# Kernel optimization log

Measured on AMD Instinct MI355X. Metric: run time of the kernel, lower is better.

## Reference

```python
import jax, jax.numpy as jnp
import numpy as np

NUM_TOKENS = 8192
EMBED_DIM = 32
BETA = 1.0
DECAY = 0.99
L2_EPS = 1e-12  # torch F.normalize denom clamp


def l2norm(t):
    return t / jnp.maximum(jnp.linalg.norm(t, axis=-1, keepdims=True), L2_EPS)


def setup_inputs() -> dict:
    key = jax.random.key(0)
    k1, k2 = jax.random.split(key)
    z = jax.random.normal(k1, (32, EMBED_DIM, 16, 16), dtype=jnp.float32)  # [B, C, H, W]
    embedding = l2norm(jax.random.normal(k2, (NUM_TOKENS, EMBED_DIM), dtype=jnp.float32))
    cluster_sizes = jnp.zeros((NUM_TOKENS,), dtype=jnp.float32)
    return {"z": z, "embedding": embedding, "cluster_sizes": cluster_sizes}


def reference(z, embedding, cluster_sizes):
    B, C, H, W = z.shape
    zc = jnp.transpose(z, (0, 2, 3, 1))          # channel_last: [B, H, W, C]
    zn = l2norm(zc)
    z_flat = zn.reshape(-1, C)                   # [N, C], N = B*H*W

    # nearest centroid by cosine similarity (codebook rows are unit norm)
    cos_sim = z_flat @ embedding.T               # [N, K]
    token_ids = jnp.argmax(cos_sim, axis=-1)     # [N]
    z_q_flat = embedding[token_ids]              # gather, [N, C]
    z_q = z_q_flat.reshape(zn.shape)

    # EMA statistics (training branch; one-hot @ matmuls expressed as scatter-adds)
    bins = jnp.zeros((NUM_TOKENS,), z.dtype).at[token_ids].add(1.0)      # encodings.sum(0)
    new_cluster_sizes = cluster_sizes * DECAY + (1.0 - DECAY) * bins
    zero_mask = bins == 0
    bins_c = jnp.where(zero_mask, 1.0, bins)
    embed_sum = jnp.zeros((NUM_TOKENS, C), z.dtype).at[token_ids].add(z_flat)  # (z_flat.T @ onehot).T
    embed_normalized = l2norm(embed_sum / bins_c[:, None])
    embed_normalized = jnp.where(zero_mask[:, None], embedding, embed_normalized)
    new_embedding = l2norm(embedding * DECAY + (1.0 - DECAY) * embed_normalized)

    # commitment loss + straight-through estimator
    loss = BETA * jnp.mean((jax.lax.stop_gradient(z_q) - zn) ** 2)
    z_q_st = zn + jax.lax.stop_gradient(z_q - zn)
    z_q_out = jnp.transpose(z_q_st, (0, 3, 1, 2))  # back to [B, C, H, W]

    return (z_q_out, loss, token_ids.reshape(B, H, W), new_embedding, new_cluster_sizes)
```

## Files before the change

### kernel.cpp

```cpp
#include <hip/hip_runtime.h>


#define NTOK   8192
#define NCODE  8192
#define CDIM   32
#define HW     256
#define DECAYF 0.99f
#define EPSF   0.01f

#define OUT_ZQ   0
#define OUT_LOSS 262144
#define OUT_IDS  262145
#define OUT_EMB  270337
#define OUT_CS   532481

#define WS_ZN     0u
#define WS_ZNBF   1048576u
#define WS_EBF    1572864u
#define WS_PMAX   2097152u
#define WS_PACK   3145728u

#define CHUNK  256
#define NCHUNK (NCODE / CHUNK)
#define TILES  (CHUNK / 16)

typedef __attribute__((ext_vector_type(8))) short bf16x8;
typedef __attribute__((ext_vector_type(4))) float f32x4;

__device__ inline unsigned short f2bf(float x) {
    unsigned u = __float_as_uint(x);
    return (unsigned short)((u + 0x7FFFu + ((u >> 16) & 1u)) >> 16);
}
__device__ inline unsigned fmap(float s) {
    unsigned u = __float_as_uint(s);
    return (u & 0x80000000u) ? ~u : (u | 0x80000000u);
}

__device__ inline void stage_chunk(const unsigned short* __restrict__ ebf,
                                   int kbase, float4* lbs5, int t) {
    const float4* src = (const float4*)(ebf + (size_t)kbase * CDIM);
#pragma unroll
    for (int j = 0; j < 4; ++j) {
        int u = t + j * 256;
        int row = u >> 2, seg = u & 3;
        lbs5[row * 5 + seg] = src[u];
    }
}

__global__ __launch_bounds__(256) void k_prep(const float* __restrict__ z,
                                              const float* __restrict__ emb,
                                              float* __restrict__ zn,
                                              unsigned short* __restrict__ znbf,
                                              unsigned short* __restrict__ ebf,
                                              unsigned long long* __restrict__ packed,
                                              float* __restrict__ out) {
    int bid = blockIdx.x, t = threadIdx.x;
    if (bid < 32) {
        int n = bid * 256 + t;
        int b = n >> 8, hw = n & 255;
        const float* zp = z + (size_t)b * (CDIM * HW) + hw;
        float v[CDIM];
        float ss = 0.f;
#pragma unroll
        for (int c = 0; c < CDIM; ++c) {
            float tv = zp[c * HW];
            v[c] = tv;
            ss += tv * tv;
        }
        float d = fmaxf(sqrtf(ss), 1e-12f);
        float* o = zn + (size_t)n * CDIM;
        unsigned short* ob = znbf + (size_t)n * CDIM;
#pragma unroll
        for (int c = 0; c < CDIM; ++c) {
            float tv = v[c] / d;
            o[c] = tv;
            ob[c] = f2bf(tv);
        }
    } else if (bid < 160) {
        int base = (bid - 32) * 2048 + t * 8;
        const float4* s = (const float4*)(emb + base);
        float4 x4 = s[0], y4 = s[1];
        ushort4 u0 = {f2bf(x4.x), f2bf(x4.y), f2bf(x4.z), f2bf(x4.w)};
        ushort4 u1 = {f2bf(y4.x), f2bf(y4.y), f2bf(y4.z), f2bf(y4.w)};
        *(ushort4*)(ebf + base) = u0;
        *(ushort4*)(ebf + base + 4) = u1;
    } else if (bid < 164) {
        int base = (bid - 160) * 2048 + t;
#pragma unroll
        for (int j = 0; j < 8; ++j) packed[base + j * 256] = 0ull;
    } else {
        if (t == 0) out[OUT_LOSS] = 0.f;
    }
}

__global__ __launch_bounds__(256) void k_max(const unsigned short* __restrict__ znbf,
                                             const unsigned short* __restrict__ ebf,
                                             float* __restrict__ pmax) {
    __shared__ float4 lbs5[CHUNK * 5];
    __shared__ float lmax[256];
    int kbase = blockIdx.y * CHUNK;
    stage_chunk(ebf, kbase, lbs5, threadIdx.x);
    __syncthreads();

    int wave = threadIdx.x >> 6, lane = threadIdx.x & 63;
    int col = lane & 15, quad = lane >> 4;
    int wtok = blockIdx.x * 256 + wave * 64;

    bf16x8 a[4];
#pragma unroll
    for (int f = 0; f < 4; ++f)
        a[f] = *(const bf16x8*)(znbf + (size_t)(wtok + f * 16 + col) * CDIM + quad * 8);

    const bf16x8* bl = (const bf16x8*)lbs5;
    const f32x4 zero4 = {0.f, 0.f, 0.f, 0.f};
    float m[4][4];
#pragma unroll
    for (int f = 0; f < 4; ++f)
#pragma unroll
        for (int r = 0; r < 4; ++r) m[f][r] = -1e30f;

    for (int t = 0; t < TILES; ++t) {
        bf16x8 b = bl[(t * 16 + col) * 5 + quad];
#pragma unroll
        for (int f = 0; f < 4; ++f) {
            f32x4 d = __builtin_amdgcn_mfma_f32_16x16x32_bf16(a[f], b, zero4, 0, 0, 0);
#pragma unroll
            for (int r = 0; r < 4; ++r) m[f][r] = fmaxf(m[f][r], d[r]);
        }
    }
#pragma unroll
    for (int f = 0; f < 4; ++f)
#pragma unroll
        for (int r = 0; r < 4; ++r) {
            float v = m[f][r];
#pragma unroll
            for (int s = 1; s < 16; s <<= 1) v = fmaxf(v, __shfl_xor(v, s));
            if (col == 0) lmax[wave * 64 + f * 16 + quad * 4 + r] = v;
        }
    __syncthreads();
    pmax[(size_t)blockIdx.y * NTOK + blockIdx.x * 256 + threadIdx.x] = lmax[threadIdx.x];
}

__global__ __launch_bounds__(256, 4) void k_pick(const float* __restrict__ zn,
                                                 const float* __restrict__ emb,
                                                 const float* __restrict__ pmax,
                                                 unsigned long long* __restrict__ packed) {
    __shared__ int qlist[256];
    __shared__ int qcnt;
    int t = threadIdx.x, lane = t & 63;
    int x = blockIdx.x, y = blockIdx.y;
    int code = y * CHUNK + t;

    if (t == 0) qcnt = 0;

    const float4* ef = (const float4*)(emb + (size_t)code * CDIM);
    float4 e0 = ef[0], e1 = ef[1], e2 = ef[2], e3 = ef[3];
    float4 e4 = ef[4], e5 = ef[5], e6 = ef[6], e7 = ef[7];

    int tok = x * 256 + t;
    float mx = -1e30f, pmy = -1e30f;
#pragma unroll
    for (int ch = 0; ch < NCHUNK; ++ch) {
        float p = pmax[(size_t)ch * NTOK + tok];
        if (ch == y) pmy = p;
        mx = fmaxf(mx, p);
    }
    __syncthreads();
    if (pmy >= mx - EPSF) qlist[atomicAdd(&qcnt, 1)] = t;
    __syncthreads();
    int nq = qcnt;

    for (int i = 0; i < nq; ++i) {
        int tl = __builtin_amdgcn_readfirstlane(qlist[i]);
        int n = x * 256 + tl;
        const float* zp = zn + (size_t)n * CDIM;
        float a0 = zp[0] * e0.x, a1 = zp[1] * e0.y;
        float a2 = zp[2] * e0.z, a3 = zp[3] * e0.w;
        a0 = __builtin_fmaf(zp[4], e1.x, a0);  a1 = __builtin_fmaf(zp[5], e1.y, a1);
        a2 = __builtin_fmaf(zp[6], e1.z, a2);  a3 = __builtin_fmaf(zp[7], e1.w, a3);
        a0 = __builtin_fmaf(zp[8], e2.x, a0);  a1 = __builtin_fmaf(zp[9], e2.y, a1);
        a2 = __builtin_fmaf(zp[10], e2.z, a2); a3 = __builtin_fmaf(zp[11], e2.w, a3);
        a0 = __builtin_fmaf(zp[12], e3.x, a0); a1 = __builtin_fmaf(zp[13], e3.y, a1);
        a2 = __builtin_fmaf(zp[14], e3.z, a2); a3 = __builtin_fmaf(zp[15], e3.w, a3);
        a0 = __builtin_fmaf(zp[16], e4.x, a0); a1 = __builtin_fmaf(zp[17], e4.y, a1);
        a2 = __builtin_fmaf(zp[18], e4.z, a2); a3 = __builtin_fmaf(zp[19], e4.w, a3);
        a0 = __builtin_fmaf(zp[20], e5.x, a0); a1 = __builtin_fmaf(zp[21], e5.y, a1);
        a2 = __builtin_fmaf(zp[22], e5.z, a2); a3 = __builtin_fmaf(zp[23], e5.w, a3);
        a0 = __builtin_fmaf(zp[24], e6.x, a0); a1 = __builtin_fmaf(zp[25], e6.y, a1);
        a2 = __builtin_fmaf(zp[26], e6.z, a2); a3 = __builtin_fmaf(zp[27], e6.w, a3);
        a0 = __builtin_fmaf(zp[28], e7.x, a0); a1 = __builtin_fmaf(zp[29], e7.y, a1);
        a2 = __builtin_fmaf(zp[30], e7.z, a2); a3 = __builtin_fmaf(zp[31], e7.w, a3);
        float s = (a0 + a1) + (a2 + a3);
        unsigned long long key = ((unsigned long long)fmap(s) << 13) |
                                 (unsigned long long)(8191 - code);
#pragma unroll
        for (int sh = 1; sh < 64; sh <<= 1) {
            unsigned long long o = __shfl_xor(key, sh);
            if (o > key) key = o;
        }
        if (lane == 0) atomicMax(packed + n, key);
    }
}

__global__ __launch_bounds__(256) void k_final(const unsigned long long* __restrict__ packed,
                                               const float* __restrict__ zn,
                                               const float* __restrict__ emb,
                                               const float* __restrict__ cs,
                                               float* __restrict__ out) {
    __shared__ float lesum[32][32];
    __shared__ int lbins[32];
    __shared__ int lsid[32];
    __shared__ float ls4[4];

    int blk = blockIdx.x, t = threadIdx.x;
    int wave = t >> 6, lane = t & 63;
    int tok0 = blk * 32, kbase = blk * 32;

    if (t < 32) lbins[t] = 0;
#pragma unroll
    for (int i = 0; i < 4; ++i) {
        int idx = i * 256 + t;
        lesum[idx >> 5][idx & 31] = 0.f;
    }
    if (t < 32) {
        int n = tok0 + t;
        int id = 8191 - (int)(packed[n] & 8191ull);
        lsid[t] = id;
        out[OUT_IDS + n] = (float)id;
    }
    __syncthreads();

    float s = 0.f;
#pragma unroll
    for (int i = 0; i < 4; ++i) {
        int idx = i * 256 + t;
        int tl = idx >> 5, c = idx & 31;
        int n = tok0 + tl;
        int id = lsid[tl];
        float ev = emb[(size_t)id * CDIM + c];
        float zv = zn[(size_t)n * CDIM + c];
        int b = n >> 8, hw = n & 255;
        out[OUT_ZQ + ((size_t)b * CDIM + c) * HW + hw] = ev;
        float dd = ev - zv;
        s += dd * dd;
    }
#pragma unroll
    for (int off = 32; off > 0; off >>= 1) s += __shfl_down(s, off);
    if (lane == 0) ls4[wave] = s;
    __syncthreads();
    if (t == 0)
        atomicAdd(out + OUT_LOSS,
                  (ls4[0] + ls4[1] + ls4[2] + ls4[3]) * (1.0f / 262144.0f));

    for (int i = 0; i < 32; ++i) {
        int n = i * 256 + t;
        int id = 8191 - (int)(packed[n] & 8191ull);
        unsigned kl = (unsigned)(id - kbase);
        if (kl < 32u) {
            atomicAdd(&lbins[kl], 1);
            const float* zp = zn + (size_t)n * CDIM;
#pragma unroll
            for (int c = 0; c < CDIM; ++c)
                atomicAdd(&lesum[kl][c], zp[c]);
        }
    }
    __syncthreads();

#pragma unroll
    for (int i = 0; i < 4; ++i) {
        int idx = i * 256 + t;
        int kl = idx >> 5, c = idx & 31;
        int k = kbase + kl;
        int bi = lbins[kl];
        float bf = (float)bi;
        bool zero = (bi == 0);
        float tv = lesum[kl][c] / (zero ? 1.0f : bf);
        float ss = tv * tv;
#pragma unroll
        for (int sh = 1; sh < 32; sh <<= 1) ss += __shfl_xor(ss, sh);
        float d = fmaxf(sqrtf(ss), 1e-12f);
        float ew = emb[(size_t)k * CDIM + c];
        float en = zero ? ew : (tv / d);
        float w = ew * DECAYF + (1.0f - DECAYF) * en;
        float ss2 = w * w;
#pragma unroll
        for (int sh = 1; sh < 32; sh <<= 1) ss2 += __shfl_xor(ss2, sh);
        float d2 = fmaxf(sqrtf(ss2), 1e-12f);
        out[OUT_EMB + (size_t)k * CDIM + c] = w / d2;
        if (c == 0) out[OUT_CS + k] = cs[k] * DECAYF + (1.0f - DECAYF) * bf;
    }
}

extern "C" void kernel_launch(void* const* d_in, const int* in_sizes, int n_in,
                              void* d_out, int out_size, void* d_ws, size_t ws_size,
                              hipStream_t stream) {
    const float* z   = (const float*)d_in[0];
    const float* emb = (const float*)d_in[1];
    const float* cs  = (const float*)d_in[2];
    float* out = (float*)d_out;
    char* ws = (char*)d_ws;

    float* zn                  = (float*)(ws + WS_ZN);
    unsigned short* znbf       = (unsigned short*)(ws + WS_ZNBF);
    unsigned short* ebf        = (unsigned short*)(ws + WS_EBF);
    float* pmax                = (float*)(ws + WS_PMAX);
    unsigned long long* packed = (unsigned long long*)(ws + WS_PACK);

    k_prep<<<dim3(165), 256, 0, stream>>>(z, emb, zn, znbf, ebf, packed, out);
    k_max<<<dim3(NTOK / 256, NCHUNK), 256, 0, stream>>>(znbf, ebf, pmax);
    k_pick<<<dim3(NTOK / 256, NCHUNK), 256, 0, stream>>>(zn, emb, pmax, packed);
    k_final<<<dim3(256), 256, 0, stream>>>(packed, zn, emb, cs, out);
}
```

Baseline: 123.8 us.

## Fuse prep kernel into k_max, converting z and codebook to bf16 in-block

Removes the separate k_prep launch. Each k_max block now normalizes its 256 tokens from z, packs them to bf16 in shared memory as MFMA A-fragments, and converts its fp32 codebook chunk to bf16 while staging. Blocks with y==0 also write the fp32 zn, zero the packed array and reset the loss. This saves a launch and the intermediate bf16 buffers, but every block redoes the token normalization and the strided z read, and reads the codebook as fp32, which doubles that traffic.

```diff
diff --git a/kernel.cpp b/kernel.cpp
--- a/kernel.cpp
+++ b/kernel.cpp
@@ -15,10 +15,8 @@
 #define OUT_CS   532481
 
 #define WS_ZN     0u
-#define WS_ZNBF   1048576u
-#define WS_EBF    1572864u
-#define WS_PMAX   2097152u
-#define WS_PACK   3145728u
+#define WS_PMAX   1048576u
+#define WS_PACK   2097152u
 
 #define CHUNK  256
 #define NCHUNK (NCODE / CHUNK)
@@ -35,28 +33,30 @@
     unsigned u = __float_as_uint(s);
     return (u & 0x80000000u) ? ~u : (u | 0x80000000u);
 }
-
-__device__ inline void stage_chunk(const unsigned short* __restrict__ ebf,
-                                   int kbase, float4* lbs5, int t) {
-    const float4* src = (const float4*)(ebf + (size_t)kbase * CDIM);
-#pragma unroll
-    for (int j = 0; j < 4; ++j) {
-        int u = t + j * 256;
-        int row = u >> 2, seg = u & 3;
-        lbs5[row * 5 + seg] = src[u];
-    }
-}
-
-__global__ __launch_bounds__(256) void k_prep(const float* __restrict__ z,
-                                              const float* __restrict__ emb,
-                                              float* __restrict__ zn,
-                                              unsigned short* __restrict__ znbf,
-                                              unsigned short* __restrict__ ebf,
-                                              unsigned long long* __restrict__ packed,
-                                              float* __restrict__ out) {
-    int bid = blockIdx.x, t = threadIdx.x;
-    if (bid < 32) {
-        int n = bid * 256 + t;
+__device__ inline float4 pack8bf(float4 p, float4 q) {
+    unsigned w0 = (unsigned)f2bf(p.x) | ((unsigned)f2bf(p.y) << 16);
+    unsigned w1 = (unsigned)f2bf(p.z) | ((unsigned)f2bf(p.w) << 16);
+    unsigned w2 = (unsigned)f2bf(q.x) | ((unsigned)f2bf(q.y) << 16);
+    unsigned w3 = (unsigned)f2bf(q.z) | ((unsigned)f2bf(q.w) << 16);
+    float4 o;
+    o.x = __uint_as_float(w0); o.y = __uint_as_float(w1);
+    o.z = __uint_as_float(w2); o.w = __uint_as_float(w3);
+    return o;
+}
+
+__global__ __launch_bounds__(256) void k_max(const float* __restrict__ z,
+                                             const float* __restrict__ emb,
+                                             float* __restrict__ zn,
+                                             float* __restrict__ pmax,
+                                             unsigned long long* __restrict__ packed,
+                                             float* __restrict__ out) {
+    __shared__ float4 lbuf[CHUNK * 5];
+    __shared__ float lmax[256];
+    int x = blockIdx.x, y = blockIdx.y, t = threadIdx.x;
+    int tok0 = x * 256;
+
+    {
+        int n = tok0 + t;
         int b = n >> 8, hw = n & 255;
         const float* zp = z + (size_t)b * (CDIM * HW) + hw;
         float v[CDIM];
@@ -68,50 +68,49 @@
             ss += tv * tv;
         }
         float d = fmaxf(sqrtf(ss), 1e-12f);
-        float* o = zn + (size_t)n * CDIM;
-        unsigned short* ob = znbf + (size_t)n * CDIM;
-#pragma unroll
-        for (int c = 0; c < CDIM; ++c) {
-            float tv = v[c] / d;
-            o[c] = tv;
-            ob[c] = f2bf(tv);
-        }
-    } else if (bid < 160) {
-        int base = (bid - 32) * 2048 + t * 8;
-        const float4* s = (const float4*)(emb + base);
-        float4 x4 = s[0], y4 = s[1];
-        ushort4 u0 = {f2bf(x4.x), f2bf(x4.y), f2bf(x4.z), f2bf(x4.w)};
-        ushort4 u1 = {f2bf(y4.x), f2bf(y4.y), f2bf(y4.z), f2bf(y4.w)};
-        *(ushort4*)(ebf + base) = u0;
-        *(ushort4*)(ebf + base + 4) = u1;
-    } else if (bid < 164) {
-        int base = (bid - 160) * 2048 + t;
-#pragma unroll
-        for (int j = 0; j < 8; ++j) packed[base + j * 256] = 0ull;
-    } else {
-        if (t == 0) out[OUT_LOSS] = 0.f;
-    }
-}
-
-__global__ __launch_bounds__(256) void k_max(const unsigned short* __restrict__ znbf,
-                                             const unsigned short* __restrict__ ebf,
-                                             float* __restrict__ pmax) {
-    __shared__ float4 lbs5[CHUNK * 5];
-    __shared__ float lmax[256];
-    int kbase = blockIdx.y * CHUNK;
-    stage_chunk(ebf, kbase, lbs5, threadIdx.x);
-    __syncthreads();
-
-    int wave = threadIdx.x >> 6, lane = threadIdx.x & 63;
+#pragma unroll
+        for (int c = 0; c < CDIM; ++c) v[c] /= d;
+        if (y == 0) {
+            float* o = zn + (size_t)n * CDIM;
+#pragma unroll
+            for (int c = 0; c < CDIM; ++c) o[c] = v[c];
+            packed[n] = 0ull;
+            if (x == 0 && t == 0) out[OUT_LOSS] = 0.f;
+        }
+#pragma unroll
+        for (int s = 0; s < 4; ++s) {
+            float4 p = {v[8 * s + 0], v[8 * s + 1], v[8 * s + 2], v[8 * s + 3]};
+            float4 q = {v[8 * s + 4], v[8 * s + 5], v[8 * s + 6], v[8 * s + 7]};
+            lbuf[t * 5 + s] = pack8bf(p, q);
+        }
+    }
+    __syncthreads();
+
+    int wave = t >> 6, lane = t & 63;
     int col = lane & 15, quad = lane >> 4;
-    int wtok = blockIdx.x * 256 + wave * 64;
 
     bf16x8 a[4];
-#pragma unroll
-    for (int f = 0; f < 4; ++f)
-        a[f] = *(const bf16x8*)(znbf + (size_t)(wtok + f * 16 + col) * CDIM + quad * 8);
-
-    const bf16x8* bl = (const bf16x8*)lbs5;
+    {
+        const bf16x8* la = (const bf16x8*)lbuf;
+#pragma unroll
+        for (int f = 0; f < 4; ++f)
+            a[f] = la[(wave * 64 + f * 16 + col) * 5 + quad];
+    }
+    __syncthreads();
+
+    {
+        int kbase = y * CHUNK;
+        const float4* src = (const float4*)(emb + (size_t)kbase * CDIM);
+#pragma unroll
+        for (int j = 0; j < 4; ++j) {
+            int u = t + j * 256;
+            float4 p = src[u * 2], q = src[u * 2 + 1];
+            lbuf[(u >> 2) * 5 + (u & 3)] = pack8bf(p, q);
+        }
+    }
+    __syncthreads();
+
+    const bf16x8* bl = (const bf16x8*)lbuf;
     const f32x4 zero4 = {0.f, 0.f, 0.f, 0.f};
     float m[4][4];
 #pragma unroll
@@ -119,8 +118,8 @@
 #pragma unroll
         for (int r = 0; r < 4; ++r) m[f][r] = -1e30f;
 
-    for (int t = 0; t < TILES; ++t) {
-        bf16x8 b = bl[(t * 16 + col) * 5 + quad];
+    for (int tt = 0; tt < TILES; ++tt) {
+        bf16x8 b = bl[(tt * 16 + col) * 5 + quad];
 #pragma unroll
         for (int f = 0; f < 4; ++f) {
             f32x4 d = __builtin_amdgcn_mfma_f32_16x16x32_bf16(a[f], b, zero4, 0, 0, 0);
@@ -138,7 +137,7 @@
             if (col == 0) lmax[wave * 64 + f * 16 + quad * 4 + r] = v;
         }
     __syncthreads();
-    pmax[(size_t)blockIdx.y * NTOK + blockIdx.x * 256 + threadIdx.x] = lmax[threadIdx.x];
+    pmax[(size_t)y * NTOK + tok0 + t] = lmax[t];
 }
 
 __global__ __launch_bounds__(256, 4) void k_pick(const float* __restrict__ zn,
@@ -301,13 +300,10 @@
     char* ws = (char*)d_ws;
 
     float* zn                  = (float*)(ws + WS_ZN);
-    unsigned short* znbf       = (unsigned short*)(ws + WS_ZNBF);
-    unsigned short* ebf        = (unsigned short*)(ws + WS_EBF);
     float* pmax                = (float*)(ws + WS_PMAX);
     unsigned long long* packed = (unsigned long long*)(ws + WS_PACK);
 
-    k_prep<<<dim3(165), 256, 0, stream>>>(z, emb, zn, znbf, ebf, packed, out);
-    k_max<<<dim3(NTOK / 256, NCHUNK), 256, 0, stream>>>(znbf, ebf, pmax);
+    k_max<<<dim3(NTOK / 256, NCHUNK), 256, 0, stream>>>(z, emb, zn, pmax, packed, out);
     k_pick<<<dim3(NTOK / 256, NCHUNK), 256, 0, stream>>>(zn, emb, pmax, packed);
     k_final<<<dim3(256), 256, 0, stream>>>(packed, zn, emb, cs, out);
 }
```

After: 128.1 us. +3.5%, slower.
